# Optimization experiments

Measured on AMD Instinct MI355X. Metric: run time of the kernel, lower is better.

The kernel has to match this reference:

```python
import jax, jax.numpy as jnp
import numpy as np

B, N, DIM = 2, 512, 256
H, DH = 8, 32
INNER = H * DH        # 256
EDGE_DIM = DIM        # default(edge_dim, dim)
SCALE = DH ** -0.5


def setup_inputs() -> dict:
    key = jax.random.key(0)
    ks = jax.random.split(key, 12)
    s = 0.02
    f32 = jnp.float32
    nodes = jax.random.normal(ks[0], (B, N, DIM), f32)
    edges = jax.random.normal(ks[1], (B, N, N, EDGE_DIM), f32)
    Wq  = jax.random.normal(ks[2], (DIM, INNER), f32) * s
    bq  = jax.random.normal(ks[3], (INNER,), f32) * s
    Wkv = jax.random.normal(ks[4], (DIM, 2 * INNER), f32) * s
    bkv = jax.random.normal(ks[5], (2 * INNER,), f32) * s
    We  = jax.random.normal(ks[6], (EDGE_DIM, INNER), f32) * s
    be  = jax.random.normal(ks[7], (INNER,), f32) * s
    Wo  = jax.random.normal(ks[8], (INNER, DIM), f32) * s
    bo  = jax.random.normal(ks[9], (DIM,), f32) * s
    return {"nodes": nodes, "edges": edges, "Wq": Wq, "bq": bq,
            "Wkv": Wkv, "bkv": bkv, "We": We, "be": be, "Wo": Wo, "bo": bo}


def reference(nodes, edges, Wq, bq, Wkv, bkv, We, be, Wo, bo):
    b, n, _ = nodes.shape
    # projections
    q = (nodes @ Wq + bq).reshape(b, n, H, DH).transpose(0, 2, 1, 3)   # b h i d
    kv = nodes @ Wkv + bkv
    k, v = jnp.split(kv, 2, axis=-1)
    k = k.reshape(b, n, H, DH).transpose(0, 2, 1, 3)                   # b h j d
    v = v.reshape(b, n, H, DH).transpose(0, 2, 1, 3)                   # b h j d
    e = (edges @ We + be).reshape(b, n, n, H, DH).transpose(0, 3, 1, 2, 4)  # b h i j d
    # sim = q . (k + e)  — split to avoid materializing k broadcast; same math
    sim = (jnp.einsum('bhid,bhjd->bhij', q, k)
           + jnp.einsum('bhid,bhijd->bhij', q, e)) * SCALE
    attn = jax.nn.softmax(sim, axis=-1)
    # out = attn . (v + e)
    out = (jnp.einsum('bhij,bhjd->bhid', attn, v)
           + jnp.einsum('bhij,bhijd->bhid', attn, e))
    out = out.transpose(0, 2, 1, 3).reshape(b, n, INNER)               # b n (h d)
    return out @ Wo + bo
```

## Files before the change

### kernel.cpp

```cpp
#include <hip/hip_runtime.h>
#include <hip/hip_bf16.h>
#include <stdint.h>

#define NB 2
#define NN 512
#define NDIM 256
#define NH 8
#define NDH 32
#define SCALE 0.17677669529663687f

__global__ __launch_bounds__(256) void k_proj(
    const float* __restrict__ nodes, const float* __restrict__ Wq, const float* __restrict__ bq,
    const float* __restrict__ Wkv, const float* __restrict__ bkv,
    const float* __restrict__ We, const float* __restrict__ be,
    float* __restrict__ q, float* __restrict__ k, float* __restrict__ v,
    float* __restrict__ qe, float* __restrict__ qbe)
{
    const int row = blockIdx.x;
    const int t = threadIdx.x;
    __shared__ float xs[NDIM];
    __shared__ float qs[NDIM];
    xs[t] = nodes[(size_t)row*NDIM + t];
    __syncthreads();

    float accq = bq[t];
    float acck = bkv[t];
    float accv = bkv[t + NDIM];
    #pragma unroll 4
    for (int d = 0; d < NDIM; ++d) {
        float x = xs[d];
        accq += x * Wq[(size_t)d*NDIM + t];
        acck += x * Wkv[(size_t)d*2*NDIM + t];
        accv += x * Wkv[(size_t)d*2*NDIM + t + NDIM];
    }
    q[(size_t)row*NDIM + t] = accq;
    k[(size_t)row*NDIM + t] = acck;
    v[(size_t)row*NDIM + t] = accv;
    qs[t] = accq;
    __syncthreads();

    float qacc[NH];
    #pragma unroll
    for (int h = 0; h < NH; ++h) qacc[h] = 0.f;
    const float* wrow = We + (size_t)t*NDIM;
    #pragma unroll
    for (int h = 0; h < NH; ++h) {
        float a0 = 0.f, a1 = 0.f, a2 = 0.f, a3 = 0.f;
        #pragma unroll
        for (int d4 = 0; d4 < NDH/4; ++d4) {
            float4 w4 = *(const float4*)(wrow + h*NDH + d4*4);
            const float* qp = qs + h*NDH + d4*4;
            a0 += qp[0]*w4.x; a1 += qp[1]*w4.y; a2 += qp[2]*w4.z; a3 += qp[3]*w4.w;
        }
        qacc[h] = (a0+a1)+(a2+a3);
    }
    #pragma unroll
    for (int h = 0; h < NH; ++h) qe[((size_t)row*NH + h)*NDIM + t] = qacc[h];
    if (t < NH) {
        float a = 0.f;
        #pragma unroll 4
        for (int d = 0; d < NDH; ++d) a += qs[t*NDH + d]*be[t*NDH + d];
        qbe[(size_t)row*NH + t] = a;
    }
}

__global__ __launch_bounds__(256, 4) void k_attn(
    const float* __restrict__ edges,
    const float* __restrict__ We, const float* __restrict__ be,
    const float* __restrict__ Wo, const float* __restrict__ bo,
    const float* __restrict__ q, const float* __restrict__ k, const float* __restrict__ v,
    const float* __restrict__ qe, const float* __restrict__ qbe,
    float* __restrict__ out)
{
    const int row = blockIdx.x;
    const int b = row >> 9;
    const int t = threadIdx.x;
    const int gA = t & 31, sA = t >> 5;
    const int jlB = t & 31, hB = t >> 5;
    const int hC = t & 7,  cbC = t >> 3;
    const bool isv = (hC == (cbC >> 2));

    __shared__ __align__(16) float uni[2560];
    __shared__ __align__(16) float simbuf[32*9];
    __shared__ __align__(16) float pbuf[256];
    __shared__ float mh[8], lh[8], al[8];

    float* qe_s   = uni;
    float* qrow_s = uni + 2048;

    const float* Erow = edges + (size_t)row*NN*NDIM;
    const float* krow = k + (size_t)b*NN*NDIM + hB*NDH;

    float4 ea[4], eb4[4];
    {
        const float* ep0 = Erow + (size_t)sA*NDIM + gA*8;
        #pragma unroll
        for (int m = 0; m < 4; ++m) {
            ea[m]  = *(const float4*)(ep0 + (size_t)m*8*NDIM);
            eb4[m] = *(const float4*)(ep0 + (size_t)m*8*NDIM + 4);
        }
    }
    {
        const float* qp = qe + (size_t)row*(NH*NDIM) + t*8;
        float4 a0 = *(const float4*)(qp);
        float4 a1 = *(const float4*)(qp + 4);
        *(float4*)(qe_s + t*8)     = a0;
        *(float4*)(qe_s + t*8 + 4) = a1;
        qrow_s[t] = q[(size_t)row*NDIM + t];
    }
    const float qbeV = qbe[(size_t)row*NH + hB];
    float w_r[8], ov_r[8];
    #pragma unroll
    for (int r = 0; r < 8; ++r) { w_r[r] = 0.f; ov_r[r] = 0.f; }
    if (t < 8) { mh[t] = -1e30f; lh[t] = 0.f; }
    __syncthreads();

    for (int jc = 0; jc < 16; ++jc) {
        const int j0 = jc*32;
        float v32_[32];
        #pragma unroll
        for (int h = 0; h < 8; ++h) {
            const float4 qa = *(const float4*)(qe_s + h*NDIM + gA*8);
            const float4 qb = *(const float4*)(qe_s + h*NDIM + gA*8 + 4);
            #pragma unroll
            for (int m = 0; m < 4; ++m) {
                v32_[m*8+h] =
                    ea[m].x*qa.x + ea[m].y*qa.y + ea[m].z*qa.z + ea[m].w*qa.w +
                    eb4[m].x*qb.x + eb4[m].y*qb.y + eb4[m].z*qb.z + eb4[m].w*qb.w;
            }
        }
        float v16_[16];
        {
            const bool bb = (gA & 16) != 0;
            #pragma unroll
            for (int i = 0; i < 16; ++i) {
                const float lo = v32_[i], hi = v32_[i+16];
                const float ot = __shfl_xor(bb ? lo : hi, 16, 64);
                v16_[i] = (bb ? hi : lo) + ot;
            }
        }
        float v8_[8];
        {
            const bool bb = (gA & 8) != 0;
            #pragma unroll
            for (int i = 0; i < 8; ++i) {
                const float lo = v16_[i], hi = v16_[i+8];
                const float ot = __shfl_xor(bb ? lo : hi, 8, 64);
                v8_[i] = (bb ? hi : lo) + ot;
            }
        }
        float v4_[4];
        {
            const bool bb = (gA & 4) != 0;
            #pragma unroll
            for (int i = 0; i < 4; ++i) {
                const float lo = v8_[i], hi = v8_[i+4];
                const float ot = __shfl_xor(bb ? lo : hi, 4, 64);
                v4_[i] = (bb ? hi : lo) + ot;
            }
        }
        float v2_[2];
        {
            const bool bb = (gA & 2) != 0;
            #pragma unroll
            for (int i = 0; i < 2; ++i) {
                const float lo = v4_[i], hi = v4_[i+2];
                const float ot = __shfl_xor(bb ? lo : hi, 2, 64);
                v2_[i] = (bb ? hi : lo) + ot;
            }
        }
        float sacc;
        {
            const bool bb = (gA & 1) != 0;
            const float lo = v2_[0], hi = v2_[1];
            const float ot = __shfl_xor(bb ? lo : hi, 1, 64);
            sacc = (bb ? hi : lo) + ot;
        }
        simbuf[(sA + (gA >> 3)*8)*9 + (gA & 7)] = sacc;
        __syncthreads();

        if (jc < 15) {
            const float* epn = Erow + (size_t)(j0 + 32 + sA)*NDIM + gA*8;
            #pragma unroll
            for (int m = 0; m < 4; ++m) {
                ea[m]  = *(const float4*)(epn + (size_t)m*8*NDIM);
                eb4[m] = *(const float4*)(epn + (size_t)m*8*NDIM + 4);
            }
        }

        {
            const int j = j0 + jlB;
            const float* kp = krow + (size_t)j*NDIM;
            const float* qp = qrow_s + hB*NDH;
            float d0=0.f,d1=0.f,d2=0.f,d3=0.f;
            #pragma unroll
            for (int u = 0; u < 8; ++u) {
                float4 kv4 = *(const float4*)(kp + u*4);
                float4 qv4 = *(const float4*)(qp + u*4);
                d0 += qv4.x*kv4.x; d1 += qv4.y*kv4.y;
                d2 += qv4.z*kv4.z; d3 += qv4.w*kv4.w;
            }
            const float sim = SCALE*(((d0+d1)+(d2+d3)) + qbeV + simbuf[jlB*9 + hB]);
            float cm = sim;
            #pragma unroll
            for (int off = 16; off >= 1; off >>= 1)
                cm = fmaxf(cm, __shfl_xor(cm, off, 64));
            const float mold = mh[hB];
            const float mnew = fmaxf(mold, cm);
            const float a_ = __expf(mold - mnew);
            const float p = __expf(sim - mnew);
            float ps = p;
            #pragma unroll
            for (int off = 16; off >= 1; off >>= 1)
                ps += __shfl_xor(ps, off, 64);
            if (jlB == 0) {
                mh[hB] = mnew;
                lh[hB] = lh[hB]*a_ + ps;
                al[hB] = a_;
            }
            pbuf[jlB*8 + hB] = p;
        }
        __syncthreads();
        {
            const float a_ = al[hC];
            #pragma unroll
            for (int r = 0; r < 8; ++r) w_r[r] *= a_;
            if (isv) {
                #pragma unroll
                for (int r = 0; r < 8; ++r) ov_r[r] *= a_;
            }
            const float* eb = Erow + (size_t)j0*NDIM + cbC*8;
            const float* vb = v + ((size_t)b*NN + j0)*NDIM + cbC*8;
            #pragma unroll 4
            for (int jl = 0; jl < 32; ++jl) {
                const float p = pbuf[jl*8 + hC];
                float4 e0 = *(const float4*)(eb + (size_t)jl*NDIM);
                float4 e1 = *(const float4*)(eb + (size_t)jl*NDIM + 4);
                w_r[0] += p*e0.x; w_r[1] += p*e0.y; w_r[2] += p*e0.z; w_r[3] += p*e0.w;
                w_r[4] += p*e1.x; w_r[5] += p*e1.y; w_r[6] += p*e1.z; w_r[7] += p*e1.w;
                if (isv) {
                    float4 v0 = *(const float4*)(vb + (size_t)jl*NDIM);
                    float4 v1 = *(const float4*)(vb + (size_t)jl*NDIM + 4);
                    ov_r[0] += p*v0.x; ov_r[1] += p*v0.y; ov_r[2] += p*v0.z; ov_r[3] += p*v0.w;
                    ov_r[4] += p*v1.x; ov_r[5] += p*v1.y; ov_r[6] += p*v1.z; ov_r[7] += p*v1.w;
                }
            }
        }
    }

    float* wfull  = uni;
    float* ovfull = uni + 2048;
    float* oibuf  = uni + 2304;
    #pragma unroll
    for (int r = 0; r < 8; ++r) wfull[hC*NDIM + cbC*8 + r] = w_r[r];
    if (isv) {
        #pragma unroll
        for (int r = 0; r < 8; ++r) ovfull[cbC*8 + r] = ov_r[r];
    }
    __syncthreads();
    {
        const int u = t, hu = u >> 5;
        const float linv = 1.f/lh[hu];
        const float* wrow = wfull + hu*NDIM;
        float a0=0.f,a1=0.f,a2=0.f,a3=0.f;
        #pragma unroll 2
        for (int c = 0; c < NDIM; c += 4) {
            a0 += wrow[c+0]*We[(size_t)(c+0)*NDIM + u];
            a1 += wrow[c+1]*We[(size_t)(c+1)*NDIM + u];
            a2 += wrow[c+2]*We[(size_t)(c+2)*NDIM + u];
            a3 += wrow[c+3]*We[(size_t)(c+3)*NDIM + u];
        }
        oibuf[u] = (ovfull[u] + ((a0+a1)+(a2+a3)))*linv + be[u];
    }
    __syncthreads();
    {
        const int u = t;
        float a0=bo[u],a1=0.f,a2=0.f,a3=0.f;
        #pragma unroll 2
        for (int x = 0; x < NDIM; x += 4) {
            a0 += oibuf[x+0]*Wo[(size_t)(x+0)*NDIM + u];
            a1 += oibuf[x+1]*Wo[(size_t)(x+1)*NDIM + u];
            a2 += oibuf[x+2]*Wo[(size_t)(x+2)*NDIM + u];
            a3 += oibuf[x+3]*Wo[(size_t)(x+3)*NDIM + u];
        }
        out[(size_t)row*NDIM + u] = (a0+a1)+(a2+a3);
    }
}

extern "C" void kernel_launch(void* const* d_in, const int* in_sizes, int n_in,
                              void* d_out, int out_size, void* d_ws, size_t ws_size,
                              hipStream_t stream) {
    const float* nodes = (const float*)d_in[0];
    const float* edges = (const float*)d_in[1];
    const float* Wq  = (const float*)d_in[2];
    const float* bq  = (const float*)d_in[3];
    const float* Wkv = (const float*)d_in[4];
    const float* bkv = (const float*)d_in[5];
    const float* We  = (const float*)d_in[6];
    const float* be  = (const float*)d_in[7];
    const float* Wo  = (const float*)d_in[8];
    const float* bo  = (const float*)d_in[9];
    (void)in_sizes; (void)n_in; (void)out_size; (void)ws_size;

    float* ws  = (float*)d_ws;
    float* q   = ws;
    float* k   = q  + 262144;
    float* v   = k  + 262144;
    float* qe  = v  + 262144;
    float* qbe = qe + 2097152;

    k_proj<<<dim3(NB*NN), dim3(256), 0, stream>>>(nodes, Wq, bq, Wkv, bkv, We, be,
                                                  q, k, v, qe, qbe);
    k_attn<<<dim3(NB*NN), dim3(256), 0, stream>>>(edges, We, be, Wo, bo,
                                                  q, k, v, qe, qbe,
                                                  (float*)d_out);
}
```

Before: 1.022 ms.

## Remap attn-times-edge accumulation to per-channel threads; process two rows per projection block

The weighted edge/value accumulation now gives each thread one channel across all eight heads, instead of eight channels for one head. Each thread reads a single scalar of edges and v per j and broadcasts the probability row from shared memory with float4 loads, padded to stride 12. This removes the divergent isv branch and spreads the v work evenly, but makes the edge reads scalar rather than float4. The projection kernel also computes two rows per block so each weight load is reused twice, halving the grid.

```diff
diff --git a/kernel.cpp b/kernel.cpp
--- a/kernel.cpp
+++ b/kernel.cpp
@@ -16,51 +16,56 @@
     float* __restrict__ q, float* __restrict__ k, float* __restrict__ v,
     float* __restrict__ qe, float* __restrict__ qbe)
 {
-    const int row = blockIdx.x;
+    const int row0 = blockIdx.x * 2;
     const int t = threadIdx.x;
-    __shared__ float xs[NDIM];
-    __shared__ float qs[NDIM];
-    xs[t] = nodes[(size_t)row*NDIM + t];
-    __syncthreads();
-
-    float accq = bq[t];
-    float acck = bkv[t];
-    float accv = bkv[t + NDIM];
-    #pragma unroll 4
+    __shared__ float xs[2][NDIM];
+    __shared__ float qs[2][NDIM];
+    xs[0][t] = nodes[(size_t)row0*NDIM + t];
+    xs[1][t] = nodes[(size_t)(row0+1)*NDIM + t];
+    __syncthreads();
+
+    float accq0 = bq[t],        accq1 = bq[t];
+    float acck0 = bkv[t],       acck1 = bkv[t];
+    float accv0 = bkv[t+NDIM],  accv1 = bkv[t+NDIM];
+    #pragma unroll 8
     for (int d = 0; d < NDIM; ++d) {
-        float x = xs[d];
-        accq += x * Wq[(size_t)d*NDIM + t];
-        acck += x * Wkv[(size_t)d*2*NDIM + t];
-        accv += x * Wkv[(size_t)d*2*NDIM + t + NDIM];
-    }
-    q[(size_t)row*NDIM + t] = accq;
-    k[(size_t)row*NDIM + t] = acck;
-    v[(size_t)row*NDIM + t] = accv;
-    qs[t] = accq;
-    __syncthreads();
-
-    float qacc[NH];
-    #pragma unroll
-    for (int h = 0; h < NH; ++h) qacc[h] = 0.f;
+        const float w0 = Wq [(size_t)d*NDIM + t];
+        const float w1 = Wkv[(size_t)d*2*NDIM + t];
+        const float w2 = Wkv[(size_t)d*2*NDIM + t + NDIM];
+        const float x0 = xs[0][d], x1 = xs[1][d];
+        accq0 += x0*w0; accq1 += x1*w0;
+        acck0 += x0*w1; acck1 += x1*w1;
+        accv0 += x0*w2; accv1 += x1*w2;
+    }
+    q[(size_t)row0*NDIM + t] = accq0;  q[(size_t)(row0+1)*NDIM + t] = accq1;
+    k[(size_t)row0*NDIM + t] = acck0;  k[(size_t)(row0+1)*NDIM + t] = acck1;
+    v[(size_t)row0*NDIM + t] = accv0;  v[(size_t)(row0+1)*NDIM + t] = accv1;
+    qs[0][t] = accq0; qs[1][t] = accq1;
+    __syncthreads();
+
     const float* wrow = We + (size_t)t*NDIM;
     #pragma unroll
     for (int h = 0; h < NH; ++h) {
-        float a0 = 0.f, a1 = 0.f, a2 = 0.f, a3 = 0.f;
+        float a0 = 0.f, a1 = 0.f, b0 = 0.f, b1 = 0.f;
         #pragma unroll
         for (int d4 = 0; d4 < NDH/4; ++d4) {
             float4 w4 = *(const float4*)(wrow + h*NDH + d4*4);
-            const float* qp = qs + h*NDH + d4*4;
-            a0 += qp[0]*w4.x; a1 += qp[1]*w4.y; a2 += qp[2]*w4.z; a3 += qp[3]*w4.w;
-        }
-        qacc[h] = (a0+a1)+(a2+a3);
-    }
-    #pragma unroll
-    for (int h = 0; h < NH; ++h) qe[((size_t)row*NH + h)*NDIM + t] = qacc[h];
-    if (t < NH) {
+            const float* qp0 = &qs[0][h*NDH + d4*4];
+            const float* qp1 = &qs[1][h*NDH + d4*4];
+            a0 += qp0[0]*w4.x + qp0[1]*w4.y;
+            a1 += qp0[2]*w4.z + qp0[3]*w4.w;
+            b0 += qp1[0]*w4.x + qp1[1]*w4.y;
+            b1 += qp1[2]*w4.z + qp1[3]*w4.w;
+        }
+        qe[((size_t)row0*NH + h)*NDIM + t]     = a0 + a1;
+        qe[((size_t)(row0+1)*NH + h)*NDIM + t] = b0 + b1;
+    }
+    if (t < 2*NH) {
+        const int r = t >> 3, h = t & 7;
         float a = 0.f;
         #pragma unroll 4
-        for (int d = 0; d < NDH; ++d) a += qs[t*NDH + d]*be[t*NDH + d];
-        qbe[(size_t)row*NH + t] = a;
+        for (int d = 0; d < NDH; ++d) a += qs[r][h*NDH + d]*be[h*NDH + d];
+        qbe[(size_t)(row0+r)*NH + h] = a;
     }
 }
 
@@ -77,13 +82,13 @@
     const int t = threadIdx.x;
     const int gA = t & 31, sA = t >> 5;
     const int jlB = t & 31, hB = t >> 5;
-    const int hC = t & 7,  cbC = t >> 3;
-    const bool isv = (hC == (cbC >> 2));
+    const int hOwn = t >> 5;
 
     __shared__ __align__(16) float uni[2560];
     __shared__ __align__(16) float simbuf[32*9];
-    __shared__ __align__(16) float pbuf[256];
-    __shared__ float mh[8], lh[8], al[8];
+    __shared__ __align__(16) float pbuf[32*12];
+    __shared__ float mh[8], lh[8];
+    __shared__ __align__(16) float al[8];
 
     float* qe_s   = uni;
     float* qrow_s = uni + 2048;
@@ -109,9 +114,10 @@
         qrow_s[t] = q[(size_t)row*NDIM + t];
     }
     const float qbeV = qbe[(size_t)row*NH + hB];
-    float w_r[8], ov_r[8];
+    float w_r[8];
+    float ov_r = 0.f;
     #pragma unroll
-    for (int r = 0; r < 8; ++r) { w_r[r] = 0.f; ov_r[r] = 0.f; }
+    for (int r = 0; r < 8; ++r) w_r[r] = 0.f;
     if (t < 8) { mh[t] = -1e30f; lh[t] = 0.f; }
     __syncthreads();
 
@@ -218,32 +224,27 @@
                 lh[hB] = lh[hB]*a_ + ps;
                 al[hB] = a_;
             }
-            pbuf[jlB*8 + hB] = p;
+            pbuf[jlB*12 + hB] = p;
         }
         __syncthreads();
         {
-            const float a_ = al[hC];
-            #pragma unroll
-            for (int r = 0; r < 8; ++r) w_r[r] *= a_;
-            if (isv) {
-                #pragma unroll
-                for (int r = 0; r < 8; ++r) ov_r[r] *= a_;
-            }
-            const float* eb = Erow + (size_t)j0*NDIM + cbC*8;
-            const float* vb = v + ((size_t)b*NN + j0)*NDIM + cbC*8;
-            #pragma unroll 4
+            const float4 al0 = *(const float4*)(al);
+            const float4 al1 = *(const float4*)(al + 4);
+            w_r[0]*=al0.x; w_r[1]*=al0.y; w_r[2]*=al0.z; w_r[3]*=al0.w;
+            w_r[4]*=al1.x; w_r[5]*=al1.y; w_r[6]*=al1.z; w_r[7]*=al1.w;
+            ov_r *= al[hOwn];
+            const float* eb = Erow + (size_t)j0*NDIM + t;
+            const float* vb = v + ((size_t)b*NN + j0)*NDIM + t;
+            #pragma unroll 8
             for (int jl = 0; jl < 32; ++jl) {
-                const float p = pbuf[jl*8 + hC];
-                float4 e0 = *(const float4*)(eb + (size_t)jl*NDIM);
-                float4 e1 = *(const float4*)(eb + (size_t)jl*NDIM + 4);
-                w_r[0] += p*e0.x; w_r[1] += p*e0.y; w_r[2] += p*e0.z; w_r[3] += p*e0.w;
-                w_r[4] += p*e1.x; w_r[5] += p*e1.y; w_r[6] += p*e1.z; w_r[7] += p*e1.w;
-                if (isv) {
-                    float4 v0 = *(const float4*)(vb + (size_t)jl*NDIM);
-                    float4 v1 = *(const float4*)(vb + (size_t)jl*NDIM + 4);
-                    ov_r[0] += p*v0.x; ov_r[1] += p*v0.y; ov_r[2] += p*v0.z; ov_r[3] += p*v0.w;
-                    ov_r[4] += p*v1.x; ov_r[5] += p*v1.y; ov_r[6] += p*v1.z; ov_r[7] += p*v1.w;
-                }
+                const float ee = eb[(size_t)jl*NDIM];
+                const float vv = vb[(size_t)jl*NDIM];
+                const float4 p0 = *(const float4*)(pbuf + jl*12);
+                const float4 p1 = *(const float4*)(pbuf + jl*12 + 4);
+                const float pv = pbuf[jl*12 + hOwn];
+                w_r[0] += p0.x*ee; w_r[1] += p0.y*ee; w_r[2] += p0.z*ee; w_r[3] += p0.w*ee;
+                w_r[4] += p1.x*ee; w_r[5] += p1.y*ee; w_r[6] += p1.z*ee; w_r[7] += p1.w*ee;
+                ov_r += pv*vv;
             }
         }
     }
@@ -252,11 +253,8 @@
     float* ovfull = uni + 2048;
     float* oibuf  = uni + 2304;
     #pragma unroll
-    for (int r = 0; r < 8; ++r) wfull[hC*NDIM + cbC*8 + r] = w_r[r];
-    if (isv) {
-        #pragma unroll
-        for (int r = 0; r < 8; ++r) ovfull[cbC*8 + r] = ov_r[r];
-    }
+    for (int h = 0; h < 8; ++h) wfull[h*NDIM + t] = w_r[h];
+    ovfull[t] = ov_r;
     __syncthreads();
     {
         const int u = t, hu = u >> 5;
@@ -309,8 +307,8 @@
     float* qe  = v  + 262144;
     float* qbe = qe + 2097152;
 
-    k_proj<<<dim3(NB*NN), dim3(256), 0, stream>>>(nodes, Wq, bq, Wkv, bkv, We, be,
-                                                  q, k, v, qe, qbe);
+    k_proj<<<dim3(NB*NN/2), dim3(256), 0, stream>>>(nodes, Wq, bq, Wkv, bkv, We, be,
+                                                    q, k, v, qe, qbe);
     k_attn<<<dim3(NB*NN), dim3(256), 0, stream>>>(edges, We, be, Wo, bo,
                                                   q, k, v, qe, qbe,
                                                   (float*)d_out);
```

New measurement: 927.6 us. 9.2% less time.
